# Kernel tuning notes

Measured on AMD Instinct MI355X. Metric: run time of the kernel, lower is better.

## Reference

```python
import jax, jax.numpy as jnp
import numpy as np

MIN_NORM = 1e-15

def mobius_add(x, y, c):
    # geoopt mobius_add with curvature k = -c (Poincare ball)
    x2 = jnp.sum(x * x, axis=-1, keepdims=True)
    y2 = jnp.sum(y * y, axis=-1, keepdims=True)
    xy = jnp.sum(x * y, axis=-1, keepdims=True)
    num = (1.0 + 2.0 * c * xy + c * y2) * x + (1.0 - c * x2) * y
    den = 1.0 + 2.0 * c * xy + c * c * x2 * y2
    return num / jnp.maximum(den, MIN_NORM)


def setup_inputs() -> dict:
    key = jax.random.key(0)
    k1, k2, k3 = jax.random.split(key, 3)
    B, D, K = 4096, 128, 256
    # points in the Poincare ball (norm << 1)
    x = jax.random.normal(k1, (B, D), jnp.float32) * 0.01
    # p_k = expmap0(randn*1e-5) ~= randn*1e-5 for tiny norms
    p_k = jax.random.normal(k2, (K, D), jnp.float32) * 1e-5
    stdv = (6.0 / (K + D)) ** 0.5
    a_k = jax.random.uniform(k3, (K, D), jnp.float32, -stdv, stdv)
    return {"x": x, "p_k": p_k, "a_k": a_k}


def reference(x, p_k, a_k):
    c = 1.0
    sqrt_c = c ** 0.5
    xq = x[:, None, :]                       # (B, 1, D)
    mpx = mobius_add(-p_k, xq, c)            # (B, K, D)
    mpx_sqnorm = jnp.maximum(jnp.sum(mpx * mpx, axis=-1), MIN_NORM)  # (B, K)
    mpx_dot_a = jnp.sum(mpx * a_k, axis=-1)                          # (B, K)
    a_norm = jnp.maximum(jnp.linalg.norm(a_k, axis=-1), MIN_NORM)    # (K,)
    num = 2.0 * sqrt_c * mpx_dot_a
    den = jnp.maximum((1.0 - c * mpx_sqnorm) * a_norm, MIN_NORM)
    distance = jnp.arcsinh(num / den) / sqrt_c
    return 2.0 * a_norm * distance           # (B, K) logits
```

## Files before the change

kernel.cpp:

```cpp
#include <hip/hip_runtime.h>
#include <hip/hip_bf16.h>
#include <math.h>

#define B_SZ 4096
#define D_SZ 128
#define K_SZ 256
#define MT   32
#define NT   32
#define LSTR 136
#define MIN_NORM 1e-15f

typedef __attribute__((ext_vector_type(8))) short  short8;
typedef __attribute__((ext_vector_type(4))) float  floatx4;

static __device__ __forceinline__ unsigned short f2bf(float f) {
    union { float f; unsigned int u; } v; v.f = f;
    unsigned int u = v.u;
    u += 0x7FFFu + ((u >> 16) & 1u);
    return (unsigned short)(u >> 16);
}
static __device__ __forceinline__ float bf2f(unsigned short h) {
    union { unsigned int u; float f; } v; v.u = ((unsigned int)h) << 16;
    return v.f;
}

__global__ __launch_bounds__(256) void mobius_mlr_kernel(
        const float* __restrict__ x, const float* __restrict__ p,
        const float* __restrict__ a, float* __restrict__ out) {
    __shared__ __align__(16) unsigned short lx[MT * LSTR];
    __shared__ __align__(16) unsigned short lp[NT * LSTR];
    __shared__ __align__(16) unsigned short la[NT * LSTR];
    __shared__ float xsq[MT];
    __shared__ float p2s[NT], pas[NT], ans[NT];

    const int tid = threadIdx.x;
    const int mb0 = blockIdx.x * MT;
    const int nb0 = blockIdx.y * NT;

    const float4* xg = (const float4*)x + (size_t)mb0 * (D_SZ / 4);
    const float4* pg = (const float4*)p + (size_t)nb0 * (D_SZ / 4);
    const float4* ag = (const float4*)a + (size_t)nb0 * (D_SZ / 4);
    #pragma unroll
    for (int j = 0; j < 4; ++j) {
        int idx = tid + j * 256;
        int row = idx >> 5;
        int c4  = idx & 31;
        float4 vx = xg[idx];
        float4 vp = pg[idx];
        float4 va = ag[idx];
        *(ushort4*)&lx[row * LSTR + c4 * 4] =
            make_ushort4(f2bf(vx.x), f2bf(vx.y), f2bf(vx.z), f2bf(vx.w));
        *(ushort4*)&lp[row * LSTR + c4 * 4] =
            make_ushort4(f2bf(vp.x), f2bf(vp.y), f2bf(vp.z), f2bf(vp.w));
        *(ushort4*)&la[row * LSTR + c4 * 4] =
            make_ushort4(f2bf(va.x), f2bf(va.y), f2bf(va.z), f2bf(va.w));
    }
    __syncthreads();

    if (tid < 128) {
        int row = tid >> 2, q = tid & 3;
        const short8* r = (const short8*)&lx[row * LSTR + q * 32];
        float s = 0.f;
        #pragma unroll
        for (int i = 0; i < 4; ++i) {
            short8 v = r[i];
            #pragma unroll
            for (int e = 0; e < 8; ++e) { float f = bf2f((unsigned short)v[e]); s += f * f; }
        }
        s += __shfl_xor(s, 1);
        s += __shfl_xor(s, 2);
        if (q == 0) xsq[row] = s;
    } else {
        int t = tid - 128;
        int row = t >> 2, q = t & 3;
        const short8* rp = (const short8*)&lp[row * LSTR + q * 32];
        const short8* ra = (const short8*)&la[row * LSTR + q * 32];
        float sp = 0.f, spa = 0.f, sa2 = 0.f;
        #pragma unroll
        for (int i = 0; i < 4; ++i) {
            short8 vp = rp[i], va = ra[i];
            #pragma unroll
            for (int e = 0; e < 8; ++e) {
                float fp = bf2f((unsigned short)vp[e]);
                float fa = bf2f((unsigned short)va[e]);
                sp += fp * fp; spa += fp * fa; sa2 += fa * fa;
            }
        }
        sp  += __shfl_xor(sp, 1);  sp  += __shfl_xor(sp, 2);
        spa += __shfl_xor(spa, 1); spa += __shfl_xor(spa, 2);
        sa2 += __shfl_xor(sa2, 1); sa2 += __shfl_xor(sa2, 2);
        if (q == 0) {
            p2s[row] = sp; pas[row] = spa;
            ans[row] = fmaxf(sqrtf(sa2), MIN_NORM);
        }
    }

    const int lane = tid & 63;
    const int wv   = tid >> 6;
    const int mi   = wv & 1;
    const int ni   = wv >> 1;
    const int quad = lane >> 4;
    const int r16  = lane & 15;

    floatx4 accp = {0.f, 0.f, 0.f, 0.f};
    floatx4 acca = {0.f, 0.f, 0.f, 0.f};
    #pragma unroll
    for (int dc = 0; dc < 4; ++dc) {
        int d0 = dc * 32 + quad * 8;
        short8 af = *(const short8*)&lx[(mi * 16 + r16) * LSTR + d0];
        short8 bp = *(const short8*)&lp[(ni * 16 + r16) * LSTR + d0];
        short8 ba = *(const short8*)&la[(ni * 16 + r16) * LSTR + d0];
        accp = __builtin_amdgcn_mfma_f32_16x16x32_bf16(af, bp, accp, 0, 0, 0);
        acca = __builtin_amdgcn_mfma_f32_16x16x32_bf16(af, ba, acca, 0, 0, 0);
    }
    __syncthreads();

    const int coll = ni * 16 + r16;
    const float p2v = p2s[coll];
    const float pav = pas[coll];
    const float anv = ans[coll];
    #pragma unroll
    for (int r = 0; r < 4; ++r) {
        int rowl = mi * 16 + quad * 4 + r;
        float x2v = xsq[rowl];
        float pdx = accp[r];
        float xda = acca[r];
        float alpha = 1.0f - 2.0f * pdx + x2v;
        float beta  = 1.0f - p2v;
        float den   = fmaxf(1.0f - 2.0f * pdx + p2v * x2v, MIN_NORM);
        float invd  = __builtin_amdgcn_rcpf(den);
        float sqn   = (alpha * alpha * p2v - 2.0f * alpha * beta * pdx
                       + beta * beta * x2v) * invd * invd;
        sqn = fmaxf(sqn, MIN_NORM);
        float mda  = (beta * xda - alpha * pav) * invd;
        float dden = fmaxf((1.0f - sqn) * anv, MIN_NORM);
        float z    = 2.0f * mda * __builtin_amdgcn_rcpf(dden);
        float dist = __logf(z + sqrtf(z * z + 1.0f));
        out[(size_t)(mb0 + rowl) * K_SZ + (nb0 + coll)] = 2.0f * anv * dist;
    }
}

extern "C" void kernel_launch(void* const* d_in, const int* in_sizes, int n_in,
                              void* d_out, int out_size, void* d_ws, size_t ws_size,
                              hipStream_t stream) {
    const float* x = (const float*)d_in[0];
    const float* p = (const float*)d_in[1];
    const float* a = (const float*)d_in[2];
    float* out = (float*)d_out;
    dim3 grid(B_SZ / MT, K_SZ / NT);
    mobius_mlr_kernel<<<grid, dim3(256), 0, stream>>>(x, p, a, out);
}
```

Before: 63.36 us.

## Load MFMA operands directly from global memory, dropping LDS staging and barriers

Each wave now computes one 16x16 output tile on its own. It reads x, p and a rows straight from global memory into registers, converts them to bf16 in-register for the MFMA, and computes the row norms and dot products with fp32 partial sums reduced by cross-lane shuffles. This removes the shared-memory staging, both __syncthreads barriers and the separate norm pass. In exchange, the reuse of x and p/a tiles across waves is lost, so there is more global/L2 traffic. The norms are also now computed from fp32 inputs rather than bf16-rounded values.

```diff
diff --git a/kernel.cpp b/kernel.cpp
--- a/kernel.cpp
+++ b/kernel.cpp
@@ -5,138 +5,90 @@
 #define B_SZ 4096
 #define D_SZ 128
 #define K_SZ 256
-#define MT   32
-#define NT   32
-#define LSTR 136
 #define MIN_NORM 1e-15f
 
 typedef __attribute__((ext_vector_type(8))) short  short8;
 typedef __attribute__((ext_vector_type(4))) float  floatx4;
 
-static __device__ __forceinline__ unsigned short f2bf(float f) {
-    union { float f; unsigned int u; } v; v.f = f;
-    unsigned int u = v.u;
-    u += 0x7FFFu + ((u >> 16) & 1u);
-    return (unsigned short)(u >> 16);
+static __device__ __forceinline__ short8 cvt8(float4 a, float4 b) {
+    union { short8 s; __hip_bfloat162 h[4]; } u;
+    u.h[0] = __float22bfloat162_rn(make_float2(a.x, a.y));
+    u.h[1] = __float22bfloat162_rn(make_float2(a.z, a.w));
+    u.h[2] = __float22bfloat162_rn(make_float2(b.x, b.y));
+    u.h[3] = __float22bfloat162_rn(make_float2(b.z, b.w));
+    return u.s;
 }
-static __device__ __forceinline__ float bf2f(unsigned short h) {
-    union { unsigned int u; float f; } v; v.u = ((unsigned int)h) << 16;
-    return v.f;
+static __device__ __forceinline__ float dot4(float4 a, float4 b) {
+    return a.x * b.x + a.y * b.y + a.z * b.z + a.w * b.w;
 }
 
 __global__ __launch_bounds__(256) void mobius_mlr_kernel(
         const float* __restrict__ x, const float* __restrict__ p,
         const float* __restrict__ a, float* __restrict__ out) {
-    __shared__ __align__(16) unsigned short lx[MT * LSTR];
-    __shared__ __align__(16) unsigned short lp[NT * LSTR];
-    __shared__ __align__(16) unsigned short la[NT * LSTR];
-    __shared__ float xsq[MT];
-    __shared__ float p2s[NT], pas[NT], ans[NT];
-
-    const int tid = threadIdx.x;
-    const int mb0 = blockIdx.x * MT;
-    const int nb0 = blockIdx.y * NT;
-
-    const float4* xg = (const float4*)x + (size_t)mb0 * (D_SZ / 4);
-    const float4* pg = (const float4*)p + (size_t)nb0 * (D_SZ / 4);
-    const float4* ag = (const float4*)a + (size_t)nb0 * (D_SZ / 4);
-    #pragma unroll
-    for (int j = 0; j < 4; ++j) {
-        int idx = tid + j * 256;
-        int row = idx >> 5;
-        int c4  = idx & 31;
-        float4 vx = xg[idx];
-        float4 vp = pg[idx];
-        float4 va = ag[idx];
-        *(ushort4*)&lx[row * LSTR + c4 * 4] =
-            make_ushort4(f2bf(vx.x), f2bf(vx.y), f2bf(vx.z), f2bf(vx.w));
-        *(ushort4*)&lp[row * LSTR + c4 * 4] =
-            make_ushort4(f2bf(vp.x), f2bf(vp.y), f2bf(vp.z), f2bf(vp.w));
-        *(ushort4*)&la[row * LSTR + c4 * 4] =
-            make_ushort4(f2bf(va.x), f2bf(va.y), f2bf(va.z), f2bf(va.w));
-    }
-    __syncthreads();
-
-    if (tid < 128) {
-        int row = tid >> 2, q = tid & 3;
-        const short8* r = (const short8*)&lx[row * LSTR + q * 32];
-        float s = 0.f;
-        #pragma unroll
-        for (int i = 0; i < 4; ++i) {
-            short8 v = r[i];
-            #pragma unroll
-            for (int e = 0; e < 8; ++e) { float f = bf2f((unsigned short)v[e]); s += f * f; }
-        }
-        s += __shfl_xor(s, 1);
-        s += __shfl_xor(s, 2);
-        if (q == 0) xsq[row] = s;
-    } else {
-        int t = tid - 128;
-        int row = t >> 2, q = t & 3;
-        const short8* rp = (const short8*)&lp[row * LSTR + q * 32];
-        const short8* ra = (const short8*)&la[row * LSTR + q * 32];
-        float sp = 0.f, spa = 0.f, sa2 = 0.f;
-        #pragma unroll
-        for (int i = 0; i < 4; ++i) {
-            short8 vp = rp[i], va = ra[i];
-            #pragma unroll
-            for (int e = 0; e < 8; ++e) {
-                float fp = bf2f((unsigned short)vp[e]);
-                float fa = bf2f((unsigned short)va[e]);
-                sp += fp * fp; spa += fp * fa; sa2 += fa * fa;
-            }
-        }
-        sp  += __shfl_xor(sp, 1);  sp  += __shfl_xor(sp, 2);
-        spa += __shfl_xor(spa, 1); spa += __shfl_xor(spa, 2);
-        sa2 += __shfl_xor(sa2, 1); sa2 += __shfl_xor(sa2, 2);
-        if (q == 0) {
-            p2s[row] = sp; pas[row] = spa;
-            ans[row] = fmaxf(sqrtf(sa2), MIN_NORM);
-        }
-    }
-
+    const int tid  = threadIdx.x;
     const int lane = tid & 63;
     const int wv   = tid >> 6;
-    const int mi   = wv & 1;
-    const int ni   = wv >> 1;
+    const int w    = blockIdx.x * 4 + wv;
+    const int ct   = w & 15;
+    const int rt   = w >> 4;
+    const int r16  = lane & 15;
     const int quad = lane >> 4;
-    const int r16  = lane & 15;
+
+    const float* xrow = x + (size_t)(rt * 16 + r16) * D_SZ;
+    const float* prow = p + (size_t)(ct * 16 + r16) * D_SZ;
+    const float* arow = a + (size_t)(ct * 16 + r16) * D_SZ;
 
     floatx4 accp = {0.f, 0.f, 0.f, 0.f};
     floatx4 acca = {0.f, 0.f, 0.f, 0.f};
+    float x2 = 0.f, p2 = 0.f, pa = 0.f, a2 = 0.f;
+
     #pragma unroll
     for (int dc = 0; dc < 4; ++dc) {
-        int d0 = dc * 32 + quad * 8;
-        short8 af = *(const short8*)&lx[(mi * 16 + r16) * LSTR + d0];
-        short8 bp = *(const short8*)&lp[(ni * 16 + r16) * LSTR + d0];
-        short8 ba = *(const short8*)&la[(ni * 16 + r16) * LSTR + d0];
+        const int d0 = dc * 32 + quad * 8;
+        float4 xv0 = *(const float4*)(xrow + d0);
+        float4 xv1 = *(const float4*)(xrow + d0 + 4);
+        float4 pv0 = *(const float4*)(prow + d0);
+        float4 pv1 = *(const float4*)(prow + d0 + 4);
+        float4 av0 = *(const float4*)(arow + d0);
+        float4 av1 = *(const float4*)(arow + d0 + 4);
+
+        x2 += dot4(xv0, xv0) + dot4(xv1, xv1);
+        p2 += dot4(pv0, pv0) + dot4(pv1, pv1);
+        pa += dot4(pv0, av0) + dot4(pv1, av1);
+        a2 += dot4(av0, av0) + dot4(av1, av1);
+
+        short8 af = cvt8(xv0, xv1);
+        short8 bp = cvt8(pv0, pv1);
+        short8 ba = cvt8(av0, av1);
         accp = __builtin_amdgcn_mfma_f32_16x16x32_bf16(af, bp, accp, 0, 0, 0);
         acca = __builtin_amdgcn_mfma_f32_16x16x32_bf16(af, ba, acca, 0, 0, 0);
     }
-    __syncthreads();
 
-    const int coll = ni * 16 + r16;
-    const float p2v = p2s[coll];
-    const float pav = pas[coll];
-    const float anv = ans[coll];
+    x2 += __shfl_xor(x2, 16); x2 += __shfl_xor(x2, 32);
+    p2 += __shfl_xor(p2, 16); p2 += __shfl_xor(p2, 32);
+    pa += __shfl_xor(pa, 16); pa += __shfl_xor(pa, 32);
+    a2 += __shfl_xor(a2, 16); a2 += __shfl_xor(a2, 32);
+    const float an = fmaxf(sqrtf(a2), MIN_NORM);
+
+    const int colg = ct * 16 + r16;
     #pragma unroll
     for (int r = 0; r < 4; ++r) {
-        int rowl = mi * 16 + quad * 4 + r;
-        float x2v = xsq[rowl];
-        float pdx = accp[r];
-        float xda = acca[r];
-        float alpha = 1.0f - 2.0f * pdx + x2v;
-        float beta  = 1.0f - p2v;
-        float den   = fmaxf(1.0f - 2.0f * pdx + p2v * x2v, MIN_NORM);
-        float invd  = __builtin_amdgcn_rcpf(den);
-        float sqn   = (alpha * alpha * p2v - 2.0f * alpha * beta * pdx
-                       + beta * beta * x2v) * invd * invd;
+        const int rowl = quad * 4 + r;
+        const float x2v = __shfl(x2, rowl);
+        const float pdx = accp[r];
+        const float xda = acca[r];
+        const float alpha = 1.0f - 2.0f * pdx + x2v;
+        const float beta  = 1.0f - p2;
+        const float den   = fmaxf(1.0f - 2.0f * pdx + p2 * x2v, MIN_NORM);
+        const float invd  = __builtin_amdgcn_rcpf(den);
+        float sqn = (alpha * alpha * p2 - 2.0f * alpha * beta * pdx
+                     + beta * beta * x2v) * invd * invd;
         sqn = fmaxf(sqn, MIN_NORM);
-        float mda  = (beta * xda - alpha * pav) * invd;
-        float dden = fmaxf((1.0f - sqn) * anv, MIN_NORM);
-        float z    = 2.0f * mda * __builtin_amdgcn_rcpf(dden);
-        float dist = __logf(z + sqrtf(z * z + 1.0f));
-        out[(size_t)(mb0 + rowl) * K_SZ + (nb0 + coll)] = 2.0f * anv * dist;
+        const float mda  = (beta * xda - alpha * pa) * invd;
+        const float dden = fmaxf((1.0f - sqn) * an, MIN_NORM);
+        const float z    = 2.0f * mda * __builtin_amdgcn_rcpf(dden);
+        const float dist = __logf(z + sqrtf(z * z + 1.0f));
+        out[(size_t)(rt * 16 + rowl) * K_SZ + colg] = 2.0f * an * dist;
     }
 }
 
@@ -147,6 +99,5 @@
     const float* p = (const float*)d_in[1];
     const float* a = (const float*)d_in[2];
     float* out = (float*)d_out;
-    dim3 grid(B_SZ / MT, K_SZ / NT);
-    mobius_mlr_kernel<<<grid, dim3(256), 0, stream>>>(x, p, a, out);
+    mobius_mlr_kernel<<<dim3(1024), dim3(256), 0, stream>>>(x, p, a, out);
 }
```

Measured after the change: 69.23 us. 1.09x slower.
